# Kernel tuning notes

Hardware: AMD Instinct MI355X
Metric: run time of the kernel (lower is better)

## Reference

```python
import jax, jax.numpy as jnp
from jax import lax
import numpy as np

NBITS = 3  # PartialSumLSQ bit width


def binarize(x):
    # straight-through sign (Binarize in BNN code modifies .data -> identity STE)
    return x + lax.stop_gradient(jnp.sign(x) - x)


def lsq(y, alpha):
    # LSQ quantizer for partial sums: q = round(clamp(y/a, Qn, Qp)) * a, STE round,
    # gradient-scaled step size (forward value unaffected by g).
    Qn, Qp = -(2 ** (NBITS - 1)), 2 ** (NBITS - 1) - 1
    g = 1.0 / np.sqrt(y.size * Qp)
    a = alpha * g + lax.stop_gradient(alpha - alpha * g)
    yc = jnp.clip(y / a, Qn, Qp)
    yq = yc + lax.stop_gradient(jnp.round(yc) - yc)
    return yq * a


def split_slices(xp, cgroups):
    # xp: [B, 128*cgroups, H+2, W+2]; reproduces split_tensor_128/256/512 ordering:
    # channel group outermost, then col offset j, then row offset i.
    H, W = xp.shape[2] - 2, xp.shape[3] - 2
    sl = [xp[:, g * 128:(g + 1) * 128, i:i + H, j:j + W]
          for g in range(cgroups) for j in range(3) for i in range(3)]
    return jnp.stack(sl)  # [S, B, 128, H, W]


def psum_stage(x, w, b, alpha, cgroups):
    # emulated 3x3 binary conv: pad, split into S shifted 128-ch slices, per-slice
    # binarized 1x1 conv + bias, LSQ-quantize each partial sum, accumulate.
    xp = jnp.pad(binarize(x), ((0, 0), (0, 0), (1, 1), (1, 1)))
    xs = split_slices(xp, cgroups)                      # [S,B,128,H,W]
    y = jnp.einsum('sbchw,soc->sbohw', xs, binarize(w)) + b[:, None, :, None, None]
    return jax.vmap(lsq)(y, alpha).sum(0)               # [B,Cout,H,W]


def maxpool2(x):
    return lax.reduce_window(x, -jnp.inf, lax.max, (1, 1, 2, 2), (1, 1, 2, 2), 'VALID')


def bn(x, g, b):
    # eval-mode BatchNorm with running_mean=0, running_var=1 -> affine
    s = (1, -1) + (1,) * (x.ndim - 2)
    return x * g.reshape(s) + b.reshape(s)


def htanh(x):
    return jnp.clip(x, -1.0, 1.0)


def _forward(x, conv1_w, conv1_b, s2_w, s2_b, s2_a, s3_w, s3_b, s3_a,
             s4_w, s4_b, s4_a, s5_w, s5_b, s5_a, s6_w, s6_b, s6_a,
             bn1_g, bn1_b, bn2_g, bn2_b, bn3_g, bn3_b, bn4_g, bn4_b,
             bn5_g, bn5_b, bn6_g, bn6_b, fc1_w, fc1_b, fc2_w, fc2_b,
             fc3_w, fc3_b, fbn1_g, fbn1_b, fbn2_g, fbn2_b, fbn3_g, fbn3_b):
    # conv1: 3->128 3x3 pad1; input has 3 channels -> not binarized, weight binarized
    h = lax.conv_general_dilated(x, binarize(conv1_w), (1, 1), ((1, 1), (1, 1)),
                                 dimension_numbers=('NCHW', 'OIHW', 'NCHW'))
    h = h + conv1_b[None, :, None, None]
    h = htanh(bn(h, bn1_g, bn1_b))
    h = psum_stage(h, s2_w, s2_b, s2_a, 1)   # 128->128, 9 slices, 32x32
    h = maxpool2(h)                          # 16x16
    h = htanh(bn(h, bn2_g, bn2_b))
    h = psum_stage(h, s3_w, s3_b, s3_a, 1)   # 128->256, 9 slices
    h = htanh(bn(h, bn3_g, bn3_b))
    h = psum_stage(h, s4_w, s4_b, s4_a, 2)   # 256->256, 18 slices
    h = maxpool2(h)                          # 8x8
    h = htanh(bn(h, bn4_g, bn4_b))
    h = psum_stage(h, s5_w, s5_b, s5_a, 2)   # 256->512, 18 slices
    h = htanh(bn(h, bn5_g, bn5_b))
    h = psum_stage(h, s6_w, s6_b, s6_a, 4)   # 512->512, 36 slices
    h = maxpool2(h)                          # 4x4
    h = htanh(bn(h, bn6_g, bn6_b))
    # binarized classifier: 512*4*4 -> 1024 -> 1024 -> num_classes
    f = binarize(h.reshape(h.shape[0], -1))
    f = f @ binarize(fc1_w).T + fc1_b
    f = htanh(f * fbn1_g + fbn1_b)
    f = binarize(f) @ binarize(fc2_w).T + fc2_b
    f = htanh(f * fbn2_g + fbn2_b)
    f = binarize(f) @ binarize(fc3_w).T + fc3_b
    return f * fbn3_g + fbn3_b


def setup_inputs() -> dict:
    key = jax.random.key(0)
    ks = iter(jax.random.split(key, 80))
    def rn(shape, scale=1.0):
        return jax.random.normal(next(ks), shape, jnp.float32) * scale
    d = {}
    d['x'] = rn((64, 3, 32, 32))
    d['conv1_w'] = rn((128, 3, 3, 3), 0.1)
    d['conv1_b'] = rn((128,), 0.01)
    stages = {'s2': (9, 128), 's3': (9, 256), 's4': (18, 256),
              's5': (18, 512), 's6': (36, 512)}
    for name, (S, co) in stages.items():
        d[name + '_w'] = rn((S, co, 128), 0.1)
        d[name + '_b'] = rn((S, co), 0.01)
        d[name + '_a'] = jax.random.uniform(next(ks), (S,), jnp.float32, 0.05, 0.15)
    for i, c in zip(range(1, 7), [128, 128, 256, 256, 512, 512]):
        d[f'bn{i}_g'] = jnp.ones((c,), jnp.float32) + rn((c,), 0.01)
        d[f'bn{i}_b'] = rn((c,), 0.01)
    d['fc1_w'] = rn((1024, 512 * 16), 0.02); d['fc1_b'] = rn((1024,), 0.01)
    d['fc2_w'] = rn((1024, 1024), 0.02);     d['fc2_b'] = rn((1024,), 0.01)
    d['fc3_w'] = rn((10, 1024), 0.02);       d['fc3_b'] = rn((10,), 0.01)
    for i, c in zip(range(1, 4), [1024, 1024, 10]):
        d[f'fbn{i}_g'] = jnp.ones((c,), jnp.float32) + rn((c,), 0.01)
        d[f'fbn{i}_b'] = rn((c,), 0.01)
    return d


def reference(x, conv1_w, conv1_b, s2_w, s2_b, s2_a, s3_w, s3_b, s3_a,
              s4_w, s4_b, s4_a, s5_w, s5_b, s5_a, s6_w, s6_b, s6_a,
              bn1_g, bn1_b, bn2_g, bn2_b, bn3_g, bn3_b, bn4_g, bn4_b,
              bn5_g, bn5_b, bn6_g, bn6_b, fc1_w, fc1_b, fc2_w, fc2_b,
              fc3_w, fc3_b, fbn1_g, fbn1_b, fbn2_g, fbn2_b, fbn3_g, fbn3_b):
    return _forward(x, conv1_w, conv1_b, s2_w, s2_b, s2_a, s3_w, s3_b, s3_a,
                    s4_w, s4_b, s4_a, s5_w, s5_b, s5_a, s6_w, s6_b, s6_a,
                    bn1_g, bn1_b, bn2_g, bn2_b, bn3_g, bn3_b, bn4_g, bn4_b,
                    bn5_g, bn5_b, bn6_g, bn6_b, fc1_w, fc1_b, fc2_w, fc2_b,
                    fc3_w, fc3_b, fbn1_g, fbn1_b, fbn2_g, fbn2_b, fbn3_g, fbn3_b)
```

## Files before the change

### kernel.cpp

```cpp
#include <hip/hip_runtime.h>
#include <hip/hip_bf16.h>
#include <math.h>

typedef unsigned long long u64;

struct PrepArgs {
    const float* w[7];
    u64* out[7];
    int cnt[7];
    int mode[7];
    const float* fc1w;
    u64* fc1T;
    const float* alpha[5];
    const float* bias[5];
    int loff[5];
    int lCout[5];
    double gq[5];
    u64* wlut;
    double* czv;
    int czoff[5];
    int czS[5];
    int R1, R2, R3, R4;
};

__global__ __launch_bounds__(256)
void k_prep(PrepArgs A) {
    int gid = blockIdx.x * 256 + threadIdx.x;
    int lane = threadIdx.x & 63;
    if (gid < A.R1) {
        int wid = gid >> 6;
        int seg = 0, base = 0, pre = 0;
#pragma unroll
        for (int t = 0; t < 7; ++t) {
            if (wid >= pre) { seg = t; base = pre; }
            pre += A.cnt[t];
        }
        int li = wid - base;
        const float* p = A.w[seg] + ((size_t)li << 6);
        u64 m = __ballot(p[lane] > 0.f);
        if (lane == 0) {
            int mode = A.mode[seg];
            size_t idx = (mode == 1) ? ((size_t)(li >> 1) * 4 + (li & 1))
                       : (mode == 2) ? ((size_t)(li & 15) * 1024 + (li >> 4))
                       : (size_t)li;
            A.out[seg][idx] = m;
        }
    } else if (gid < A.R2) {
        int wid = (gid - A.R1) >> 6;
        int row = wid >> 3, gk = wid & 7;
        int g = gk >> 1, k = gk & 1;
        int c = g * 128 + k * 64 + lane;
        const float* p = A.fc1w + (size_t)row * 8192 + (size_t)c * 16;
        float arr[16];
#pragma unroll
        for (int q = 0; q < 4; ++q) {
            float4 f = ((const float4*)p)[q];
            arr[4 * q + 0] = f.x; arr[4 * q + 1] = f.y;
            arr[4 * q + 2] = f.z; arr[4 * q + 3] = f.w;
        }
#pragma unroll
        for (int h = 0; h < 4; ++h)
#pragma unroll
        for (int xq = 0; xq < 4; ++xq) {
            u64 m = __ballot(arr[h * 4 + xq] > 0.f);
            if (lane == 0) {
                int wd = g * 32 + h * 8 + xq * 2 + k;
                A.fc1T[(size_t)wd * 1024 + row] = m;
            }
        }
    } else if (gid < A.R3) {
        int idx = gid - A.R2;
        int seg = 0;
#pragma unroll
        for (int t = 1; t < 5; ++t) if (idx >= A.loff[t]) seg = t;
        int li = idx - A.loff[seg];
        int s = li / A.lCout[seg];
        double al = (double)A.alpha[seg][s];
        double tg = al * A.gq[seg];
        double a  = tg + (al - tg);
        double b  = (double)A.bias[seg][li];
        double q0 = rint(fmin(fmax(b / a, -4.0), 3.0));
        double qp = rint(fmin(fmax((2.0 + b) / a, -4.0), 3.0));
        double qn = rint(fmin(fmax((-2.0 + b) / a, -4.0), 3.0));
        double cz = q0 * a;
        A.wlut[(size_t)idx * 4 + 2] = __double_as_longlong(qp * a - cz);
        A.wlut[(size_t)idx * 4 + 3] = __double_as_longlong(qn * a - cz);
    } else if (gid < A.R4) {
        int idx = gid - A.R3;
        int seg = 0;
#pragma unroll
        for (int t = 1; t < 5; ++t) if (idx >= A.czoff[t]) seg = t;
        int o = idx - A.czoff[seg];
        int Cout = A.lCout[seg];
        double CZ = 0.0;
        for (int s = 0; s < A.czS[seg]; ++s) {
            double al = (double)A.alpha[seg][s];
            double tg = al * A.gq[seg];
            double a  = tg + (al - tg);
            double b  = (double)A.bias[seg][s * Cout + o];
            double q0 = rint(fmin(fmax(b / a, -4.0), 3.0));
            CZ += q0 * a;
        }
        A.czv[idx] = CZ;
    }
}

__global__ __launch_bounds__(128)
void k_conv1(const float* __restrict__ x, const float* __restrict__ w,
             const float* __restrict__ cb, const float* __restrict__ g1,
             const float* __restrict__ b1, u64* __restrict__ apack) {
    __shared__ double xs[3][3][34];
    int h = blockIdx.x & 31;
    int b = blockIdx.x >> 5;
    int tid = threadIdx.x;
    for (int idx = tid; idx < 306; idx += 128) {
        int dyy = idx / 102;
        int rem = idx - dyy * 102;
        int ci = rem / 34;
        int col = rem - ci * 34;
        int y = h + dyy - 1, xx = col - 1;
        double v = 0.0;
        if ((unsigned)y < 32u && (unsigned)xx < 32u)
            v = (double)x[((b * 3 + ci) * 32 + y) * 32 + xx];
        xs[dyy][ci][col] = v;
    }
    __syncthreads();
    int o = tid;
    double sg[3][3][3];
#pragma unroll
    for (int ci = 0; ci < 3; ++ci)
#pragma unroll
    for (int ky = 0; ky < 3; ++ky)
#pragma unroll
    for (int kx = 0; kx < 3; ++kx) {
        float wv = w[o * 27 + (ci * 3 + ky) * 3 + kx];
        sg[kx][ci][ky] = wv > 0.f ? 1.0 : (wv < 0.f ? -1.0 : 0.0);
    }
    double cbv = (double)cb[o], g1v = (double)g1[o], b1v = (double)b1[o];
    double A0 = 0.0, A1 = 0.0, A2 = 0.0;
    for (int pc = 0; pc < 34; ++pc) {
        double v[3][3];
#pragma unroll
        for (int ky = 0; ky < 3; ++ky)
#pragma unroll
        for (int ci = 0; ci < 3; ++ci)
            v[ky][ci] = xs[ky][ci][pc];
        A2 = 0.0;
#pragma unroll
        for (int ci = 0; ci < 3; ++ci)
#pragma unroll
        for (int ky = 0; ky < 3; ++ky) {
            A0 += v[ky][ci] * sg[2][ci][ky];
            A1 += v[ky][ci] * sg[1][ci][ky];
            A2 += v[ky][ci] * sg[0][ci][ky];
        }
        if (pc >= 2) {
            int wc = pc - 2;
            double t = (A0 + cbv) * g1v + b1v;
            u64 m = __ballot(t > 0.0);
            if ((tid & 63) == 0)
                apack[((size_t)(b * 1024 + h * 32 + wc)) * 2 + (tid >> 6)] = m;
        }
        A0 = A1; A1 = A2;
    }
}

template <int POOL, int G, int H, int W, int Cout, int RCH, int NCH>
__global__ __launch_bounds__(64 * RCH * NCH)
void k_stage(const u64* __restrict__ apack, const u64* __restrict__ wlut,
             const double* __restrict__ czv,
             const float* __restrict__ gam, const float* __restrict__ bet,
             u64* __restrict__ opack) {
    constexpr int CW = W / NCH;
    constexpr int Ho = H / POOL, Wo = W / POOL;
    constexpr int NOC = Cout / 64;
    constexpr int NRB = H / RCH;

    int bi = blockIdx.x;
    int och = bi % NOC; bi /= NOC;
    int rb = bi % NRB;
    int b = bi / NRB;
    int tid = threadIdx.x;
    int ol = tid & 63;
    int rr = tid >> 6;
    int rc = rr / NCH;
    int nc = rr - rc * NCH;
    int o = och * 64 + ol;
    int yr = rb * RCH + rc;

    double CZ = czv[o];
    double acc[CW];
#pragma unroll
    for (int c = 0; c < CW; ++c) acc[c] = CZ;

    ulonglong2 ar[CW + 2];

    for (int g = 0; g < G; ++g) {
#pragma unroll
        for (int i = 0; i < 3; ++i) {
            int y = yr + i - 1;
            if ((unsigned)y >= (unsigned)H) continue;
            const ulonglong2* rp = (const ulonglong2*)
                (apack + ((((size_t)(b * G + g) * H + y) * W + nc * CW - 1)) * 2);
#pragma unroll
            for (int k = 0; k < CW + 2; ++k) {
                if ((k > 0 || nc > 0) && (k < CW + 1 || nc < NCH - 1))
                    ar[k] = rp[k];
            }
#pragma unroll
            for (int j = 0; j < 3; ++j) {
                const int s = g * 9 + j * 3 + i;
                size_t so = (size_t)s * Cout + o;
                ulonglong2 wv = *(const ulonglong2*)(wlut + so * 4);
                ulonglong2 dv = *(const ulonglong2*)(wlut + so * 4 + 2);
                u64 w0 = wv.x, w1 = wv.y;
                double dp = __longlong_as_double(dv.x);
                double dn = __longlong_as_double(dv.y);
#pragma unroll
                for (int c = 0; c < CW; ++c) {
                    if (c == 0 && j == 0 && nc == 0) continue;
                    if (c == CW - 1 && j == 2 && nc == NCH - 1) continue;
                    u64 a0 = ar[c + j].x, a1 = ar[c + j].y;
                    int d = __popcll(a0 ^ w0) + __popcll(a1 ^ w1);
                    double val = (d < 64) ? dp : dn;
                    val = (d == 64) ? 0.0 : val;
                    acc[c] += val;
                }
            }
        }
    }

    double gv = (double)gam[o], bv = (double)bet[o];
    if constexpr (POOL == 1) {
#pragma unroll
        for (int c = 0; c < CW; ++c) {
            double t = acc[c] * gv + bv;
            u64 bm = __ballot(t > 0.0);
            if (ol == 0) {
                int pw = nc * CW + c;
                opack[(((size_t)(b * (Cout >> 7) + (o >> 7)) * Ho + yr) * Wo + pw) * 2
                      + (och & 1)] = bm;
            }
        }
    } else {
        __shared__ double pl[RCH / 2][NCH][CW / 2][64];
        double m2[CW / 2];
#pragma unroll
        for (int c2 = 0; c2 < CW / 2; ++c2)
            m2[c2] = fmax(acc[2 * c2], acc[2 * c2 + 1]);
        if (rc & 1) {
#pragma unroll
            for (int c2 = 0; c2 < CW / 2; ++c2)
                pl[rc >> 1][nc][c2][ol] = m2[c2];
        }
        __syncthreads();
        if (!(rc & 1)) {
#pragma unroll
            for (int c2 = 0; c2 < CW / 2; ++c2) {
                double m = fmax(m2[c2], pl[rc >> 1][nc][c2][ol]);
                double t = m * gv + bv;
                u64 bm = __ballot(t > 0.0);
                if (ol == 0) {
                    int ph = yr >> 1;
                    int pw = ((nc * CW) >> 1) + c2;
                    opack[(((size_t)(b * (Cout >> 7) + (o >> 7)) * Ho + ph) * Wo + pw) * 2
                          + (och & 1)] = bm;
                }
            }
        }
    }
}

__global__ __launch_bounds__(1024)
void k_fc_all(const u64* __restrict__ abits, const u64* __restrict__ wf1T,
              const float* __restrict__ b1, const float* __restrict__ g1,
              const float* __restrict__ a1,
              const u64* __restrict__ wf2T,
              const float* __restrict__ b2, const float* __restrict__ g2,
              const float* __restrict__ a2,
              const u64* __restrict__ wf3,
              const float* __restrict__ b3, const float* __restrict__ g3,
              const float* __restrict__ a3,
              float* __restrict__ out) {
    __shared__ u64 sa[128];
    __shared__ u64 sp1[16];
    __shared__ u64 sp2[16];
    int b = blockIdx.x;
    int t = threadIdx.x;
    if (t < 128) sa[t] = abits[(size_t)b * 128 + t];
    __syncthreads();
    {
        int d = 0;
#pragma unroll 16
        for (int i = 0; i < 128; ++i)
            d += __popcll(sa[i] ^ wf1T[(size_t)i * 1024 + t]);
        double isum = (double)(8192 - 2 * d);
        double v = (isum + (double)b1[t]) * (double)g1[t] + (double)a1[t];
        u64 m = __ballot(v > 0.0);
        if ((t & 63) == 0) sp1[t >> 6] = m;
    }
    __syncthreads();
    {
        int d = 0;
#pragma unroll
        for (int i = 0; i < 16; ++i)
            d += __popcll(sp1[i] ^ wf2T[(size_t)i * 1024 + t]);
        double isum = (double)(1024 - 2 * d);
        double v = (isum + (double)b2[t]) * (double)g2[t] + (double)a2[t];
        u64 m = __ballot(v > 0.0);
        if ((t & 63) == 0) sp2[t >> 6] = m;
    }
    __syncthreads();
    if (t < 10) {
        int d = 0;
#pragma unroll
        for (int i = 0; i < 16; ++i)
            d += __popcll(sp2[i] ^ wf3[t * 16 + i]);
        double isum = (double)(1024 - 2 * d);
        out[b * 10 + t] = (float)((isum + (double)b3[t]) * (double)g3[t] + (double)a3[t]);
    }
}


extern "C" void kernel_launch(void* const* d_in, const int* in_sizes, int n_in,
                              void* d_out, int out_size, void* d_ws, size_t ws_size,
                              hipStream_t stream) {
    const float* x       = (const float*)d_in[0];
    const float* conv1_w = (const float*)d_in[1];
    const float* conv1_b = (const float*)d_in[2];
    const float* s_w[5]  = {(const float*)d_in[3], (const float*)d_in[6], (const float*)d_in[9],
                            (const float*)d_in[12], (const float*)d_in[15]};
    const float* s_b[5]  = {(const float*)d_in[4], (const float*)d_in[7], (const float*)d_in[10],
                            (const float*)d_in[13], (const float*)d_in[16]};
    const float* s_a[5]  = {(const float*)d_in[5], (const float*)d_in[8], (const float*)d_in[11],
                            (const float*)d_in[14], (const float*)d_in[17]};
    const float* bn_g[6], *bn_b[6];
    for (int i = 0; i < 6; ++i) { bn_g[i] = (const float*)d_in[18 + 2 * i]; bn_b[i] = (const float*)d_in[19 + 2 * i]; }
    const float* fc1_w = (const float*)d_in[30]; const float* fc1_b = (const float*)d_in[31];
    const float* fc2_w = (const float*)d_in[32]; const float* fc2_b = (const float*)d_in[33];
    const float* fc3_w = (const float*)d_in[34]; const float* fc3_b = (const float*)d_in[35];
    const float* fbn_g[3], *fbn_b[3];
    for (int i = 0; i < 3; ++i) { fbn_g[i] = (const float*)d_in[36 + 2 * i]; fbn_b[i] = (const float*)d_in[37 + 2 * i]; }

    size_t off = 0;
    auto alloc = [&](size_t bytes) { off = (off + 255) & ~(size_t)255; size_t o = off; off += bytes; return o; };
    char* ws = (char*)d_ws;
    size_t o_apA  = alloc(1048576);
    size_t o_apB  = alloc(1048576);
    size_t o_wlut = alloc((size_t)35712 * 4 * 8);
    size_t o_cz   = alloc((size_t)1664 * 8);
    size_t o_wf1  = alloc((size_t)1024 * 128 * 8);
    size_t o_wf2  = alloc((size_t)1024 * 16 * 8);
    size_t o_wf3  = alloc((size_t)160 * 8);
    if (off > ws_size) return;

    u64* apA = (u64*)(ws + o_apA);
    u64* apB = (u64*)(ws + o_apB);
    u64* wlut = (u64*)(ws + o_wlut);
    double* czbuf = (double*)(ws + o_cz);
    u64* wf1T = (u64*)(ws + o_wf1);
    u64* wf2T = (u64*)(ws + o_wf2);
    u64* wf3 = (u64*)(ws + o_wf3);

    const int rowoff[5] = {0, 1152, 3456, 8064, 17280};
    const int czoff[5]  = {0, 128, 384, 640, 1152};
    const int sS[5]     = {9, 9, 18, 18, 36};
    const int sCout[5]  = {128, 256, 256, 512, 512};
    const double sYsz[5] = {8388608.0, 4194304.0, 4194304.0, 2097152.0, 2097152.0};

    PrepArgs PA;
    const int scnt[5] = {2304, 4608, 9216, 18432, 36864};
    int totw = 0;
    for (int i = 0; i < 5; ++i) {
        PA.w[i] = s_w[i];
        PA.out[i] = wlut + (size_t)rowoff[i] * 4;
        PA.cnt[i] = scnt[i];
        PA.mode[i] = 1;
        totw += scnt[i];
    }
    PA.w[5] = fc2_w; PA.out[5] = wf2T; PA.cnt[5] = 1024 * 16; PA.mode[5] = 2; totw += 1024 * 16;
    PA.w[6] = fc3_w; PA.out[6] = wf3;  PA.cnt[6] = 160;       PA.mode[6] = 0; totw += 160;
    PA.fc1w = fc1_w; PA.fc1T = wf1T;
    for (int i = 0; i < 5; ++i) {
        PA.alpha[i] = s_a[i]; PA.bias[i] = s_b[i];
        PA.loff[i] = rowoff[i]; PA.lCout[i] = sCout[i];
        PA.gq[i] = 1.0 / sqrt(sYsz[i] * 3.0);
        PA.czoff[i] = czoff[i]; PA.czS[i] = sS[i];
    }
    PA.wlut = wlut; PA.czv = czbuf;
    PA.R1 = totw * 64;
    PA.R2 = PA.R1 + 1024 * 8 * 64;
    PA.R3 = PA.R2 + 35712;
    PA.R4 = PA.R3 + 1664;
    k_prep<<<(PA.R4 + 255) / 256, 256, 0, stream>>>(PA);

    k_conv1<<<64 * 32, 128, 0, stream>>>(x, conv1_w, conv1_b, bn_g[0], bn_b[0], apA);

    k_stage<2, 1, 32, 32, 128, 2, 4><<<64 * 16 * 2, 512, 0, stream>>>(
        apA, wlut + (size_t)rowoff[0] * 4, czbuf + czoff[0], bn_g[1], bn_b[1], apB);
    k_stage<1, 1, 16, 16, 256, 2, 2><<<64 * 8 * 4, 256, 0, stream>>>(
        apB, wlut + (size_t)rowoff[1] * 4, czbuf + czoff[1], bn_g[2], bn_b[2], apA);
    k_stage<2, 2, 16, 16, 256, 2, 2><<<64 * 8 * 4, 256, 0, stream>>>(
        apA, wlut + (size_t)rowoff[2] * 4, czbuf + czoff[2], bn_g[3], bn_b[3], apB);
    k_stage<1, 2, 8, 8, 512, 2, 1><<<64 * 4 * 8, 128, 0, stream>>>(
        apB, wlut + (size_t)rowoff[3] * 4, czbuf + czoff[3], bn_g[4], bn_b[4], apA);
    k_stage<2, 4, 8, 8, 512, 2, 1><<<64 * 4 * 8, 128, 0, stream>>>(
        apA, wlut + (size_t)rowoff[4] * 4, czbuf + czoff[4], bn_g[5], bn_b[5], apB);

    k_fc_all<<<64, 1024, 0, stream>>>(apB, wf1T, fc1_b, fbn_g[0], fbn_b[0],
                                      wf2T, fc2_b, fbn_g[1], fbn_b[1],
                                      wf3, fc3_b, fbn_g[2], fbn_b[2],
                                      (float*)d_out);
}
```

Measured before the change: 226.7 us.

## Stage activations in LDS, branchless sign-FMA LUT, and precomputed padding corrections

Each stage block now loads its padded activation tile into shared memory once instead of every thread reading overlapping rows from global memory. The per-pixel select on the popcount result becomes a branchless sign times (mid, half) FMA, using a LUT re-encoded as mid/half. Border-pixel special cases are dropped from the inner loop and corrected afterwards with per-channel padding sums precomputed by a new k_pv kernel. This adds an extra small launch and shared-memory use, and makes correctness depend on the padding correction being exact in double arithmetic.

```diff
diff --git a/kernel.cpp b/kernel.cpp
--- a/kernel.cpp
+++ b/kernel.cpp
@@ -17,10 +17,7 @@
     int lCout[5];
     double gq[5];
     u64* wlut;
-    double* czv;
-    int czoff[5];
-    int czS[5];
-    int R1, R2, R3, R4;
+    int R1, R2, R3;
 };
 
 __global__ __launch_bounds__(256)
@@ -83,26 +80,59 @@
         double qp = rint(fmin(fmax((2.0 + b) / a, -4.0), 3.0));
         double qn = rint(fmin(fmax((-2.0 + b) / a, -4.0), 3.0));
         double cz = q0 * a;
-        A.wlut[(size_t)idx * 4 + 2] = __double_as_longlong(qp * a - cz);
-        A.wlut[(size_t)idx * 4 + 3] = __double_as_longlong(qn * a - cz);
-    } else if (gid < A.R4) {
-        int idx = gid - A.R3;
-        int seg = 0;
-#pragma unroll
-        for (int t = 1; t < 5; ++t) if (idx >= A.czoff[t]) seg = t;
-        int o = idx - A.czoff[seg];
-        int Cout = A.lCout[seg];
-        double CZ = 0.0;
-        for (int s = 0; s < A.czS[seg]; ++s) {
-            double al = (double)A.alpha[seg][s];
-            double tg = al * A.gq[seg];
-            double a  = tg + (al - tg);
-            double b  = (double)A.bias[seg][s * Cout + o];
-            double q0 = rint(fmin(fmax(b / a, -4.0), 3.0));
-            CZ += q0 * a;
-        }
-        A.czv[idx] = CZ;
-    }
+        double dp = qp * a - cz, dn = qn * a - cz;
+        A.wlut[(size_t)idx * 4 + 2] = __double_as_longlong(0.5 * (dp + dn));
+        A.wlut[(size_t)idx * 4 + 3] = __double_as_longlong(0.5 * (dp - dn));
+    }
+}
+
+struct PvArgs {
+    const float* alpha[5];
+    const float* bias[5];
+    int rowoff[5];
+    int czoff[5];
+    int S[5];
+    int Cout[5];
+    double gq[5];
+    int total;
+};
+
+__global__ void k_pv(PvArgs A, const u64* __restrict__ wlut,
+                     double* __restrict__ czv, double* __restrict__ pvt) {
+    int idx = blockIdx.x * blockDim.x + threadIdx.x;
+    if (idx >= A.total) return;
+    int seg = 0;
+#pragma unroll
+    for (int t = 1; t < 5; ++t) if (idx >= A.czoff[t]) seg = t;
+    int o = idx - A.czoff[seg];
+    int Cout = A.Cout[seg];
+    double CZ = 0.0;
+    double pv[8] = {0, 0, 0, 0, 0, 0, 0, 0};
+    for (int s = 0; s < A.S[seg]; ++s) {
+        double al = (double)A.alpha[seg][s];
+        double tg = al * A.gq[seg];
+        double a  = tg + (al - tg);
+        double b  = (double)A.bias[seg][s * Cout + o];
+        double q0 = rint(fmin(fmax(b / a, -4.0), 3.0));
+        CZ += q0 * a;
+        size_t so = (size_t)(A.rowoff[seg] + s * Cout + o);
+        const u64* wl = wlut + so * 4;
+        u64 w0 = wl[0], w1 = wl[1];
+        double mid  = __longlong_as_double(wl[2]);
+        double half = __longlong_as_double(wl[3]);
+        int e0 = 64 - (__popcll(w0) + __popcll(w1));
+        int sg = min(max(e0, -1), 1);
+        double sd = (double)sg;
+        double pvv = fma(sd, fma(mid, sd, half), 0.0);
+        int i3 = s % 3, j3 = (s / 3) % 3;
+        if (i3 == 0) { pv[0] += pvv; if (j3 == 0) pv[4] += pvv; if (j3 == 2) pv[6] += pvv; }
+        if (i3 == 2) { pv[1] += pvv; if (j3 == 0) pv[5] += pvv; if (j3 == 2) pv[7] += pvv; }
+        if (j3 == 0) pv[2] += pvv;
+        if (j3 == 2) pv[3] += pvv;
+    }
+    czv[idx] = CZ;
+#pragma unroll
+    for (int k = 0; k < 8; ++k) pvt[(size_t)idx * 8 + k] = pv[k];
 }
 
 __global__ __launch_bounds__(128)
@@ -168,13 +198,21 @@
 template <int POOL, int G, int H, int W, int Cout, int RCH, int NCH>
 __global__ __launch_bounds__(64 * RCH * NCH)
 void k_stage(const u64* __restrict__ apack, const u64* __restrict__ wlut,
-             const double* __restrict__ czv,
+             const double* __restrict__ czv, const double* __restrict__ pvt,
              const float* __restrict__ gam, const float* __restrict__ bet,
              u64* __restrict__ opack) {
     constexpr int CW = W / NCH;
     constexpr int Ho = H / POOL, Wo = W / POOL;
     constexpr int NOC = Cout / 64;
     constexpr int NRB = H / RCH;
+    constexpr int NT = 64 * RCH * NCH;
+    constexpr int NR = RCH + 2;
+    constexpr int NCOL = W + 2;
+    __shared__ alignas(16) u64 sact[G][NR][NCOL][2];
+    constexpr int PLP = (POOL == 2) ? (RCH / 2) : 1;
+    constexpr int PLN = (POOL == 2) ? NCH : 1;
+    constexpr int PLC = (POOL == 2) ? (CW / 2) : 1;
+    __shared__ double pl[PLP][PLN][PLC][64];
 
     int bi = blockIdx.x;
     int och = bi % NOC; bi /= NOC;
@@ -187,47 +225,81 @@
     int nc = rr - rc * NCH;
     int o = och * 64 + ol;
     int yr = rb * RCH + rc;
+    int c0 = nc * CW;
+
+    for (int t = tid; t < G * NR * NCOL; t += NT) {
+        int g = t / (NR * NCOL);
+        int r2 = t - g * (NR * NCOL);
+        int yy = r2 / NCOL;
+        int xx = r2 - yy * NCOL;
+        int y = rb * RCH + yy - 1;
+        int x = xx - 1;
+        u64 v0 = 0, v1 = 0;
+        if ((unsigned)y < (unsigned)H && (unsigned)x < (unsigned)W) {
+            const u64* p = apack + ((size_t)((b * G + g) * H + y) * W + x) * 2;
+            v0 = p[0]; v1 = p[1];
+        }
+        sact[g][yy][xx][0] = v0;
+        sact[g][yy][xx][1] = v1;
+    }
+    __syncthreads();
 
     double CZ = czv[o];
     double acc[CW];
 #pragma unroll
     for (int c = 0; c < CW; ++c) acc[c] = CZ;
 
-    ulonglong2 ar[CW + 2];
-
+#pragma unroll 1
     for (int g = 0; g < G; ++g) {
 #pragma unroll
         for (int i = 0; i < 3; ++i) {
-            int y = yr + i - 1;
-            if ((unsigned)y >= (unsigned)H) continue;
-            const ulonglong2* rp = (const ulonglong2*)
-                (apack + ((((size_t)(b * G + g) * H + y) * W + nc * CW - 1)) * 2);
-#pragma unroll
-            for (int k = 0; k < CW + 2; ++k) {
-                if ((k > 0 || nc > 0) && (k < CW + 1 || nc < NCH - 1))
-                    ar[k] = rp[k];
-            }
+            const int yy = rc + i;
+            ulonglong2 ar[CW + 2];
+#pragma unroll
+            for (int k = 0; k < CW + 2; ++k)
+                ar[k] = *(const ulonglong2*)&sact[g][yy][c0 + k][0];
 #pragma unroll
             for (int j = 0; j < 3; ++j) {
-                const int s = g * 9 + j * 3 + i;
+                int s = g * 9 + j * 3 + i;
                 size_t so = (size_t)s * Cout + o;
                 ulonglong2 wv = *(const ulonglong2*)(wlut + so * 4);
-                ulonglong2 dv = *(const ulonglong2*)(wlut + so * 4 + 2);
+                ulonglong2 mh = *(const ulonglong2*)(wlut + so * 4 + 2);
                 u64 w0 = wv.x, w1 = wv.y;
-                double dp = __longlong_as_double(dv.x);
-                double dn = __longlong_as_double(dv.y);
+                double mid  = __longlong_as_double(mh.x);
+                double half = __longlong_as_double(mh.y);
 #pragma unroll
                 for (int c = 0; c < CW; ++c) {
-                    if (c == 0 && j == 0 && nc == 0) continue;
-                    if (c == CW - 1 && j == 2 && nc == NCH - 1) continue;
                     u64 a0 = ar[c + j].x, a1 = ar[c + j].y;
                     int d = __popcll(a0 ^ w0) + __popcll(a1 ^ w1);
-                    double val = (d < 64) ? dp : dn;
-                    val = (d == 64) ? 0.0 : val;
-                    acc[c] += val;
+                    int e = 64 - d;
+                    int sg = min(max(e, -1), 1);
+                    double sd = (double)sg;
+                    acc[c] = fma(sd, fma(mid, sd, half), acc[c]);
                 }
             }
         }
+    }
+
+    const double* pvo = pvt + (size_t)o * 8;
+    if (yr == 0) {
+        double v = pvo[0];
+#pragma unroll
+        for (int c = 0; c < CW; ++c) acc[c] -= v;
+    }
+    if (yr == H - 1) {
+        double v = pvo[1];
+#pragma unroll
+        for (int c = 0; c < CW; ++c) acc[c] -= v;
+    }
+    if (nc == 0) {
+        acc[0] -= pvo[2];
+        if (yr == 0)     acc[0] += pvo[4];
+        if (yr == H - 1) acc[0] += pvo[5];
+    }
+    if (nc == NCH - 1) {
+        acc[CW - 1] -= pvo[3];
+        if (yr == 0)     acc[CW - 1] += pvo[6];
+        if (yr == H - 1) acc[CW - 1] += pvo[7];
     }
 
     double gv = (double)gam[o], bv = (double)bet[o];
@@ -237,13 +309,12 @@
             double t = acc[c] * gv + bv;
             u64 bm = __ballot(t > 0.0);
             if (ol == 0) {
-                int pw = nc * CW + c;
+                int pw = c0 + c;
                 opack[(((size_t)(b * (Cout >> 7) + (o >> 7)) * Ho + yr) * Wo + pw) * 2
                       + (och & 1)] = bm;
             }
         }
     } else {
-        __shared__ double pl[RCH / 2][NCH][CW / 2][64];
         double m2[CW / 2];
 #pragma unroll
         for (int c2 = 0; c2 < CW / 2; ++c2)
@@ -262,7 +333,7 @@
                 u64 bm = __ballot(t > 0.0);
                 if (ol == 0) {
                     int ph = yr >> 1;
-                    int pw = ((nc * CW) >> 1) + c2;
+                    int pw = (c0 >> 1) + c2;
                     opack[(((size_t)(b * (Cout >> 7) + (o >> 7)) * Ho + ph) * Wo + pw) * 2
                           + (och & 1)] = bm;
                 }
@@ -349,6 +420,7 @@
     size_t o_apB  = alloc(1048576);
     size_t o_wlut = alloc((size_t)35712 * 4 * 8);
     size_t o_cz   = alloc((size_t)1664 * 8);
+    size_t o_pvt  = alloc((size_t)1664 * 8 * 8);
     size_t o_wf1  = alloc((size_t)1024 * 128 * 8);
     size_t o_wf2  = alloc((size_t)1024 * 16 * 8);
     size_t o_wf3  = alloc((size_t)160 * 8);
@@ -358,6 +430,7 @@
     u64* apB = (u64*)(ws + o_apB);
     u64* wlut = (u64*)(ws + o_wlut);
     double* czbuf = (double*)(ws + o_cz);
+    double* pvbuf = (double*)(ws + o_pvt);
     u64* wf1T = (u64*)(ws + o_wf1);
     u64* wf2T = (u64*)(ws + o_wf2);
     u64* wf3 = (u64*)(ws + o_wf3);
@@ -385,27 +458,40 @@
         PA.alpha[i] = s_a[i]; PA.bias[i] = s_b[i];
         PA.loff[i] = rowoff[i]; PA.lCout[i] = sCout[i];
         PA.gq[i] = 1.0 / sqrt(sYsz[i] * 3.0);
-        PA.czoff[i] = czoff[i]; PA.czS[i] = sS[i];
-    }
-    PA.wlut = wlut; PA.czv = czbuf;
+    }
+    PA.wlut = wlut;
     PA.R1 = totw * 64;
     PA.R2 = PA.R1 + 1024 * 8 * 64;
     PA.R3 = PA.R2 + 35712;
-    PA.R4 = PA.R3 + 1664;
-    k_prep<<<(PA.R4 + 255) / 256, 256, 0, stream>>>(PA);
+    k_prep<<<(PA.R3 + 255) / 256, 256, 0, stream>>>(PA);
+
+    PvArgs VA;
+    for (int i = 0; i < 5; ++i) {
+        VA.alpha[i] = s_a[i]; VA.bias[i] = s_b[i];
+        VA.rowoff[i] = rowoff[i]; VA.czoff[i] = czoff[i];
+        VA.S[i] = sS[i]; VA.Cout[i] = sCout[i];
+        VA.gq[i] = 1.0 / sqrt(sYsz[i] * 3.0);
+    }
+    VA.total = 1664;
+    k_pv<<<(1664 + 255) / 256, 256, 0, stream>>>(VA, wlut, czbuf, pvbuf);
 
     k_conv1<<<64 * 32, 128, 0, stream>>>(x, conv1_w, conv1_b, bn_g[0], bn_b[0], apA);
 
     k_stage<2, 1, 32, 32, 128, 2, 4><<<64 * 16 * 2, 512, 0, stream>>>(
-        apA, wlut + (size_t)rowoff[0] * 4, czbuf + czoff[0], bn_g[1], bn_b[1], apB);
+        apA, wlut + (size_t)rowoff[0] * 4, czbuf + czoff[0], pvbuf + (size_t)czoff[0] * 8,
+        bn_g[1], bn_b[1], apB);
     k_stage<1, 1, 16, 16, 256, 2, 2><<<64 * 8 * 4, 256, 0, stream>>>(
-        apB, wlut + (size_t)rowoff[1] * 4, czbuf + czoff[1], bn_g[2], bn_b[2], apA);
+        apB, wlut + (size_t)rowoff[1] * 4, czbuf + czoff[1], pvbuf + (size_t)czoff[1] * 8,
+        bn_g[2], bn_b[2], apA);
     k_stage<2, 2, 16, 16, 256, 2, 2><<<64 * 8 * 4, 256, 0, stream>>>(
-        apA, wlut + (size_t)rowoff[2] * 4, czbuf + czoff[2], bn_g[3], bn_b[3], apB);
+        apA, wlut + (size_t)rowoff[2] * 4, czbuf + czoff[2], pvbuf + (size_t)czoff[2] * 8,
+        bn_g[3], bn_b[3], apB);
     k_stage<1, 2, 8, 8, 512, 2, 1><<<64 * 4 * 8, 128, 0, stream>>>(
-        apB, wlut + (size_t)rowoff[3] * 4, czbuf + czoff[3], bn_g[4], bn_b[4], apA);
+        apB, wlut + (size_t)rowoff[3] * 4, czbuf + czoff[3], pvbuf + (size_t)czoff[3] * 8,
+        bn_g[4], bn_b[4], apA);
     k_stage<2, 4, 8, 8, 512, 2, 1><<<64 * 4 * 8, 128, 0, stream>>>(
-        apA, wlut + (size_t)rowoff[4] * 4, czbuf + czoff[4], bn_g[5], bn_b[5], apB);
+        apA, wlut + (size_t)rowoff[4] * 4, czbuf + czoff[4], pvbuf + (size_t)czoff[4] * 8,
+        bn_g[5], bn_b[5], apB);
 
     k_fc_all<<<64, 1024, 0, stream>>>(apB, wf1T, fc1_b, fbn_g[0], fbn_b[0],
                                       wf2T, fc2_b, fbn_g[1], fbn_b[1],
```

After: 238.6 us. +5.2%, slower.
